# Kernel tuning notes

Measured on AMD Instinct MI355X. Metric: run time of the kernel, lower is better.

Reference implementation:

```python
import jax, jax.numpy as jnp
import numpy as np

N_PTS = 1048576
FEAT = 32
RES = 256


def _sample_plane(plane, gu, gv):
    """Bilinear grid_sample, align_corners=True.
    plane: (C, H, W); gu in [-1,1] indexes W, gv in [-1,1] indexes H.
    Returns (N, C)."""
    C, H, W = plane.shape
    px = (gu + 1.0) * 0.5 * (W - 1)
    py = (gv + 1.0) * 0.5 * (H - 1)
    x0 = jnp.floor(px)
    y0 = jnp.floor(py)
    wx = (px - x0)[None, :]
    wy = (py - y0)[None, :]
    x0i = jnp.clip(x0.astype(jnp.int32), 0, W - 1)
    x1i = jnp.clip(x0i + 1, 0, W - 1)
    y0i = jnp.clip(y0.astype(jnp.int32), 0, H - 1)
    y1i = jnp.clip(y0i + 1, 0, H - 1)
    f00 = plane[:, y0i, x0i]  # (C, N)
    f01 = plane[:, y0i, x1i]
    f10 = plane[:, y1i, x0i]
    f11 = plane[:, y1i, x1i]
    out = (f00 * (1 - wx) * (1 - wy) + f01 * wx * (1 - wy)
           + f10 * (1 - wx) * wy + f11 * wx * wy)
    return out.T  # (N, C)


def setup_inputs() -> dict:
    key = jax.random.key(0)
    ks = jax.random.split(key, 12)
    x = jax.random.uniform(ks[0], (N_PTS, 3), dtype=jnp.float32) * 2.0 - 0.5  # some outside box to exercise clamp
    d = jax.random.normal(ks[1], (N_PTS, 3), dtype=jnp.float32)
    plane_xy = jax.random.normal(ks[2], (FEAT, RES, RES), dtype=jnp.float32)
    plane_xz = jax.random.normal(ks[3], (FEAT, RES, RES), dtype=jnp.float32)
    plane_yz = jax.random.normal(ks[4], (FEAT, RES, RES), dtype=jnp.float32)
    center = jnp.zeros((3,), dtype=jnp.float32)
    scale = jnp.ones((3,), dtype=jnp.float32)
    s = 0.1
    w_sigma1 = jax.random.normal(ks[5], (3 * FEAT, 64), dtype=jnp.float32) * s
    w_sigma2 = jax.random.normal(ks[6], (64, 16), dtype=jnp.float32) * s
    w_color1 = jax.random.normal(ks[7], (15, 64), dtype=jnp.float32) * s
    w_color2 = jax.random.normal(ks[8], (64, 64), dtype=jnp.float32) * s
    w_color3 = jax.random.normal(ks[9], (64, 3), dtype=jnp.float32) * s
    return {"x": x, "d": d, "plane_xy": plane_xy, "plane_xz": plane_xz,
            "plane_yz": plane_yz, "center": center, "scale": scale,
            "w_sigma1": w_sigma1, "w_sigma2": w_sigma2,
            "w_color1": w_color1, "w_color2": w_color2, "w_color3": w_color3}


def reference(x, d, plane_xy, plane_xz, plane_yz, center, scale,
              w_sigma1, w_sigma2, w_color1, w_color2, w_color3):
    # normalize into unit cube and clamp
    xn = jnp.clip((x - center) / scale + 0.5, 0.0, 1.0)
    g = xn * 2.0 - 1.0  # (N, 3) in [-1, 1]
    gx, gy, gz = g[:, 0], g[:, 1], g[:, 2]
    # torch grid_sample: grid[...,0] indexes W (last dim), grid[...,1] indexes H
    feat_xy = _sample_plane(plane_xy, gx, gy)  # plane (C,resX,resY): W<-x, H<-y
    feat_xz = _sample_plane(plane_xz, gx, gz)
    feat_yz = _sample_plane(plane_yz, gy, gz)
    feat = jnp.concatenate([feat_xy, feat_xz, feat_yz], axis=1)  # (N, 96)
    # sigma net: 96 -> 64 (ReLU) -> 16, no bias (tcnn FullyFusedMLP)
    h = jax.nn.relu(feat @ w_sigma1)
    out16 = h @ w_sigma2  # (N, 16)
    sigma = out16[:, 0]
    # color net: 15 -> 64 -> 64 (ReLU) -> 3, sigmoid output
    c = jax.nn.relu(out16[:, 1:] @ w_color1)
    c = jax.nn.relu(c @ w_color2)
    color = jax.nn.sigmoid(c @ w_color3)
    return color, sigma
```

## Files before the change

kernel.cpp:

```cpp
#include <hip/hip_runtime.h>
#include <stdint.h>

typedef __attribute__((ext_vector_type(8))) unsigned short ushort8v;
typedef __attribute__((ext_vector_type(8))) short bf16x8;
typedef __attribute__((ext_vector_type(4))) float f32x4;
typedef __attribute__((ext_vector_type(2))) float f32x2;
typedef __attribute__((ext_vector_type(4))) unsigned int uint4v;

__device__ __forceinline__ float bf2f(unsigned short u) {
    return __uint_as_float(((unsigned)u) << 16);
}
__device__ __forceinline__ unsigned short f2bf(float f) {
    unsigned u = __float_as_uint(f);
    unsigned r = u + 0x7fffu + ((u >> 16) & 1u);
    return (unsigned short)(r >> 16);
}
__device__ __forceinline__ unsigned cvt_pk_bf16(float lo, float hi) {
    unsigned r;
    asm("v_cvt_pk_bf16_f32 %0, %1, %2" : "=v"(r) : "v"(lo), "v"(hi));
    return r;
}
__device__ __forceinline__ f32x2 up2(unsigned u) {
    f32x2 r;
    r[0] = __uint_as_float(u << 16);
    r[1] = __uint_as_float(u & 0xffff0000u);
    return r;
}

__global__ __launch_bounds__(256) void transpose_planes_kernel(
    const float* __restrict__ pxy, const float* __restrict__ pxz,
    const float* __restrict__ pyz, unsigned int* __restrict__ tp)
{
    __shared__ unsigned int lt[64 * 17];
    const int bid = blockIdx.x;
    const int plane = bid >> 10;
    const int base = (bid & 1023) * 64;
    const float* __restrict__ src = plane == 0 ? pxy : (plane == 1 ? pxz : pyz);
    const int tid = threadIdx.x;
    {
        const int c2 = tid >> 4;
        const int s  = tid & 15;
        const f32x4 va = *(const f32x4*)(src + (size_t)(2 * c2)     * 65536 + base + 4 * s);
        const f32x4 vb = *(const f32x4*)(src + (size_t)(2 * c2 + 1) * 65536 + base + 4 * s);
        #pragma unroll
        for (int j = 0; j < 4; ++j) {
            int yx = 4 * s + j;
            lt[yx * 17 + c2] = ((unsigned)f2bf(vb[j]) << 16) | (unsigned)f2bf(va[j]);
        }
    }
    __syncthreads();
    {
        const int yx = tid >> 2, q = tid & 3;
        uint4v o;
        #pragma unroll
        for (int k = 0; k < 4; ++k) o[k] = lt[yx * 17 + 4 * q + k];
        *(uint4v*)(tp + ((size_t)plane * 65536 + base + yx) * 16 + 4 * q) = o;
    }
}

__global__ __launch_bounds__(256) void pack_weights_kernel(
    const float* __restrict__ w1, const float* __restrict__ w2,
    const float* __restrict__ wc1, const float* __restrict__ wc2,
    const float* __restrict__ wc3, unsigned int* __restrict__ pack)
{
    int t = blockIdx.x * 256 + threadIdx.x;
    if (t >= 28 * 64) return;
    int lane = t & 63, tile = t >> 6;
    int mat, mt, kc;
    if (tile < 12)      { mat = 0; kc = tile >> 2;        mt = tile & 3; }
    else if (tile < 14) { mat = 1; kc = tile - 12;        mt = 0; }
    else if (tile < 18) { mat = 2; kc = 0;                mt = tile - 14; }
    else if (tile < 26) { mat = 3; kc = (tile - 18) >> 2; mt = (tile - 18) & 3; }
    else                { mat = 4; kc = tile - 26;        mt = 0; }
    int of = mt * 16 + (lane & 15);
    int kb = kc * 32 + (lane >> 4) * 8;
    float f[8];
    #pragma unroll
    for (int j = 0; j < 8; ++j) {
        int k = kb + j;
        float v;
        if (mat == 0)      v = w1[k * 64 + of];
        else if (mat == 1) v = w2[k * 16 + of];
        else if (mat == 2) v = (k >= 1 && k < 16) ? wc1[(k - 1) * 64 + of] : 0.0f;
        else if (mat == 3) v = wc2[k * 64 + of];
        else               v = (of < 3) ? wc3[k * 3 + of] : 0.0f;
        f[j] = v;
    }
    int sl = lane ^ (lane >> 3);
    unsigned int* dst = pack + tile * 256 + sl * 4;
    #pragma unroll
    for (int w = 0; w < 4; ++w)
        dst[w] = ((unsigned)f2bf(f[2 * w + 1]) << 16) | (unsigned)f2bf(f[2 * w]);
}

__global__ __launch_bounds__(512) void nerf_mfma_kernel(
    const float* __restrict__ xin,
    const unsigned short* __restrict__ tp,
    const unsigned int* __restrict__ wpack,
    const float* __restrict__ center, const float* __restrict__ scale,
    float* __restrict__ out, int npts, int nwt)
{
    __shared__ unsigned int wlds[28 * 256];
    const int tid = threadIdx.x;
    #pragma unroll 2
    for (int idx = tid; idx < 28 * 256; idx += 512) wlds[idx] = wpack[idx];
    __syncthreads();

    const int lane = tid & 63;
    const int wv   = tid >> 6;
    const int p    = lane & 15;
    const int G    = lane >> 4;
    const bool hi32 = (lane & 32) != 0;
    const int sl   = lane ^ (lane >> 3);
    const bf16x8* Af = (const bf16x8*)wlds;

    const float ctr0 = center[0], ctr1 = center[1], ctr2 = center[2];
    const float sc0 = scale[0], sc1 = scale[1], sc2 = scale[2];

    for (int wtb = blockIdx.x * 8; wtb < nwt; wtb += gridDim.x * 8) {
        asm volatile("" ::: "memory");
        const int wt = wtb + wv;
        const int gpt = wt * 16 + p;
        const bool valid = (wt < nwt) && (gpt < npts);
        const int rp = valid ? gpt : (npts - 1);
        const float xv = xin[3 * rp + 0], yv = xin[3 * rp + 1], zv = xin[3 * rp + 2];

        auto norm1 = [&](float v, float c, float s) {
            float xn = fminf(fmaxf((v - c) / s + 0.5f, 0.0f), 1.0f);
            return xn * 2.0f - 1.0f;
        };
        const float gx = norm1(xv, ctr0, sc0);
        const float gy = norm1(yv, ctr1, sc1);
        const float gz = norm1(zv, ctr2, sc2);
        const float us[3] = {gx, gx, gy};
        const float vs[3] = {gy, gz, gz};

        f32x4 acc1[4];
        #pragma unroll
        for (int mt = 0; mt < 4; ++mt) acc1[mt] = f32x4{0.f, 0.f, 0.f, 0.f};
        #pragma unroll
        for (int pl = 0; pl < 3; ++pl) {
            float pxf = (us[pl] + 1.0f) * 0.5f * 255.0f;
            float pyf = (vs[pl] + 1.0f) * 0.5f * 255.0f;
            float x0f = floorf(pxf), y0f = floorf(pyf);
            float wx = pxf - x0f, wy = pyf - y0f;
            int x0 = min(max((int)x0f, 0), 255), y0 = min(max((int)y0f, 0), 255);
            int x1 = min(x0 + 1, 255), y1 = min(y0 + 1, 255);
            float w00 = (1.f - wx) * (1.f - wy), w01 = wx * (1.f - wy);
            float w10 = (1.f - wx) * wy,         w11 = wx * wy;
            const f32x2 W00 = {w00, w00}, W01 = {w01, w01}, W10 = {w10, w10}, W11 = {w11, w11};
            const size_t pbase = ((size_t)pl << 16);
            const uint4v v00 = *(const uint4v*)(tp + (pbase + (size_t)(y0 * 256 + x0)) * 32 + G * 8);
            const uint4v v01 = *(const uint4v*)(tp + (pbase + (size_t)(y0 * 256 + x1)) * 32 + G * 8);
            const uint4v v10 = *(const uint4v*)(tp + (pbase + (size_t)(y1 * 256 + x0)) * 32 + G * 8);
            const uint4v v11 = *(const uint4v*)(tp + (pbase + (size_t)(y1 * 256 + x1)) * 32 + G * 8);
            uint4v bw;
            #pragma unroll
            for (int w = 0; w < 4; ++w) {
                f32x2 a = up2(v00[w]) * W00 + up2(v01[w]) * W01
                        + up2(v10[w]) * W10 + up2(v11[w]) * W11;
                bw[w] = cvt_pk_bf16(a[0], a[1]);
            }
            bf16x8 bfr = __builtin_bit_cast(bf16x8, bw);
            #pragma unroll
            for (int mt = 0; mt < 4; ++mt)
                acc1[mt] = __builtin_amdgcn_mfma_f32_16x16x32_bf16(
                    Af[(pl * 4 + mt) * 64 + sl], bfr, acc1[mt], 0, 0, 0);
        }

        unsigned pk1[4][2];
        #pragma unroll
        for (int mt = 0; mt < 4; ++mt) {
            pk1[mt][0] = cvt_pk_bf16(fmaxf(acc1[mt][0], 0.f), fmaxf(acc1[mt][1], 0.f));
            pk1[mt][1] = cvt_pk_bf16(fmaxf(acc1[mt][2], 0.f), fmaxf(acc1[mt][3], 0.f));
        }
        f32x4 acc2 = f32x4{0.f, 0.f, 0.f, 0.f};
        #pragma unroll
        for (int kc2 = 0; kc2 < 2; ++kc2) {
            uint4v bw;
            #pragma unroll
            for (int w = 0; w < 4; ++w) {
                int src = p + 16 * (2 * (G & 1) + (w >> 1));
                unsigned lo_ = (unsigned)__shfl((int)pk1[2 * kc2][w & 1], src, 64);
                unsigned hi_ = (unsigned)__shfl((int)pk1[2 * kc2 + 1][w & 1], src, 64);
                bw[w] = hi32 ? hi_ : lo_;
            }
            acc2 = __builtin_amdgcn_mfma_f32_16x16x32_bf16(
                Af[(12 + kc2) * 64 + sl], __builtin_bit_cast(bf16x8, bw), acc2, 0, 0, 0);
        }
        if (valid && lane < 16) out[(size_t)3 * npts + gpt] = acc2[0];

        unsigned pk2[2];
        pk2[0] = cvt_pk_bf16(acc2[0], acc2[1]);
        pk2[1] = cvt_pk_bf16(acc2[2], acc2[3]);
        uint4v bw3;
        #pragma unroll
        for (int w = 0; w < 4; ++w) {
            int src = p + 16 * (2 * (G & 1) + (w >> 1));
            unsigned v = (unsigned)__shfl((int)pk2[w & 1], src, 64);
            bw3[w] = (G < 2) ? v : 0u;
        }
        bf16x8 b3 = __builtin_bit_cast(bf16x8, bw3);
        f32x4 acc3[4];
        #pragma unroll
        for (int mt = 0; mt < 4; ++mt) acc3[mt] = f32x4{0.f, 0.f, 0.f, 0.f};
        #pragma unroll
        for (int mt = 0; mt < 4; ++mt)
            acc3[mt] = __builtin_amdgcn_mfma_f32_16x16x32_bf16(
                Af[(14 + mt) * 64 + sl], b3, acc3[mt], 0, 0, 0);

        unsigned pk3[4][2];
        #pragma unroll
        for (int mt = 0; mt < 4; ++mt) {
            pk3[mt][0] = cvt_pk_bf16(fmaxf(acc3[mt][0], 0.f), fmaxf(acc3[mt][1], 0.f));
            pk3[mt][1] = cvt_pk_bf16(fmaxf(acc3[mt][2], 0.f), fmaxf(acc3[mt][3], 0.f));
        }
        f32x4 acc4[4];
        #pragma unroll
        for (int mt = 0; mt < 4; ++mt) acc4[mt] = f32x4{0.f, 0.f, 0.f, 0.f};
        #pragma unroll
        for (int kc2 = 0; kc2 < 2; ++kc2) {
            uint4v bw;
            #pragma unroll
            for (int w = 0; w < 4; ++w) {
                int src = p + 16 * (2 * (G & 1) + (w >> 1));
                unsigned lo_ = (unsigned)__shfl((int)pk3[2 * kc2][w & 1], src, 64);
                unsigned hi_ = (unsigned)__shfl((int)pk3[2 * kc2 + 1][w & 1], src, 64);
                bw[w] = hi32 ? hi_ : lo_;
            }
            bf16x8 b = __builtin_bit_cast(bf16x8, bw);
            #pragma unroll
            for (int mt = 0; mt < 4; ++mt)
                acc4[mt] = __builtin_amdgcn_mfma_f32_16x16x32_bf16(
                    Af[(18 + kc2 * 4 + mt) * 64 + sl], b, acc4[mt], 0, 0, 0);
        }

        unsigned pk4[4][2];
        #pragma unroll
        for (int mt = 0; mt < 4; ++mt) {
            pk4[mt][0] = cvt_pk_bf16(fmaxf(acc4[mt][0], 0.f), fmaxf(acc4[mt][1], 0.f));
            pk4[mt][1] = cvt_pk_bf16(fmaxf(acc4[mt][2], 0.f), fmaxf(acc4[mt][3], 0.f));
        }
        f32x4 acc5 = f32x4{0.f, 0.f, 0.f, 0.f};
        #pragma unroll
        for (int kc2 = 0; kc2 < 2; ++kc2) {
            uint4v bw;
            #pragma unroll
            for (int w = 0; w < 4; ++w) {
                int src = p + 16 * (2 * (G & 1) + (w >> 1));
                unsigned lo_ = (unsigned)__shfl((int)pk4[2 * kc2][w & 1], src, 64);
                unsigned hi_ = (unsigned)__shfl((int)pk4[2 * kc2 + 1][w & 1], src, 64);
                bw[w] = hi32 ? hi_ : lo_;
            }
            acc5 = __builtin_amdgcn_mfma_f32_16x16x32_bf16(
                Af[(26 + kc2) * 64 + sl], __builtin_bit_cast(bf16x8, bw), acc5, 0, 0, 0);
        }
        if (valid && lane < 16) {
            out[(size_t)3 * gpt + 0] = 1.0f / (1.0f + __expf(-acc5[0]));
            out[(size_t)3 * gpt + 1] = 1.0f / (1.0f + __expf(-acc5[1]));
            out[(size_t)3 * gpt + 2] = 1.0f / (1.0f + __expf(-acc5[2]));
        }
    }
}

__global__ __launch_bounds__(256) void nerf_fallback_kernel(
    const float* __restrict__ xin,
    const float* __restrict__ pxy, const float* __restrict__ pxz,
    const float* __restrict__ pyz,
    const float* __restrict__ center, const float* __restrict__ scale,
    const float* __restrict__ w1, const float* __restrict__ w2,
    const float* __restrict__ wc1, const float* __restrict__ wc2,
    const float* __restrict__ wc3, float* __restrict__ out, int npts)
{
    __shared__ unsigned short act[64][256];
    const int tid = threadIdx.x;
    const int i = blockIdx.x * 256 + tid;
    if (i >= npts) return;
    const float xv = xin[3 * i], yv = xin[3 * i + 1], zv = xin[3 * i + 2];
    auto norm1 = [&](float v, int k) {
        float xn = fminf(fmaxf((v - center[k]) / scale[k] + 0.5f, 0.0f), 1.0f);
        return xn * 2.0f - 1.0f;
    };
    const float gx = norm1(xv, 0), gy = norm1(yv, 1), gz = norm1(zv, 2);
    float h[64];
    #pragma unroll
    for (int j = 0; j < 64; ++j) h[j] = 0.0f;
    auto samp = [&](float gu, float gv, int pl, const float* __restrict__ splane) {
        float pxf = (gu + 1.0f) * 0.5f * 255.0f, pyf = (gv + 1.0f) * 0.5f * 255.0f;
        float x0f = floorf(pxf), y0f = floorf(pyf);
        float wx = pxf - x0f, wy = pyf - y0f;
        int x0 = min(max((int)x0f, 0), 255), y0 = min(max((int)y0f, 0), 255);
        int x1 = min(x0 + 1, 255), y1 = min(y0 + 1, 255);
        float w00 = (1 - wx) * (1 - wy), w01 = wx * (1 - wy), w10 = (1 - wx) * wy, w11 = wx * wy;
        for (int c = 0; c < 32; ++c) {
            const float* b = splane + (size_t)c * 65536;
            float f = b[y0 * 256 + x0] * w00 + b[y0 * 256 + x1] * w01
                    + b[y1 * 256 + x0] * w10 + b[y1 * 256 + x1] * w11;
            const float* wr = w1 + (size_t)((pl * 32 + c) * 64);
            #pragma unroll
            for (int j = 0; j < 64; ++j) h[j] = fmaf(f, wr[j], h[j]);
        }
    };
    samp(gx, gy, 0, pxy); samp(gx, gz, 1, pxz); samp(gy, gz, 2, pyz);
    #pragma unroll
    for (int j = 0; j < 64; ++j) act[j][tid] = f2bf(fmaxf(h[j], 0.0f));
    float o[16];
    #pragma unroll
    for (int j = 0; j < 16; ++j) o[j] = 0.0f;
    for (int k = 0; k < 64; ++k) {
        float hv = bf2f(act[k][tid]);
        #pragma unroll
        for (int j = 0; j < 16; ++j) o[j] = fmaf(hv, w2[k * 16 + j], o[j]);
    }
    out[(size_t)3 * npts + i] = o[0];
    float c1[64];
    #pragma unroll
    for (int j = 0; j < 64; ++j) c1[j] = 0.0f;
    #pragma unroll
    for (int k = 0; k < 15; ++k)
        #pragma unroll
        for (int j = 0; j < 64; ++j) c1[j] = fmaf(o[k + 1], wc1[k * 64 + j], c1[j]);
    #pragma unroll
    for (int j = 0; j < 64; ++j) act[j][tid] = f2bf(fmaxf(c1[j], 0.0f));
    float c2[64];
    #pragma unroll
    for (int j = 0; j < 64; ++j) c2[j] = 0.0f;
    for (int k = 0; k < 64; ++k) {
        float v = bf2f(act[k][tid]);
        #pragma unroll
        for (int j = 0; j < 64; ++j) c2[j] = fmaf(v, wc2[k * 64 + j], c2[j]);
    }
    float r0 = 0, r1 = 0, r2 = 0;
    #pragma unroll
    for (int k = 0; k < 64; ++k) {
        float v = fmaxf(c2[k], 0.0f);
        r0 = fmaf(v, wc3[k * 3 + 0], r0);
        r1 = fmaf(v, wc3[k * 3 + 1], r1);
        r2 = fmaf(v, wc3[k * 3 + 2], r2);
    }
    out[(size_t)3 * i + 0] = 1.0f / (1.0f + expf(-r0));
    out[(size_t)3 * i + 1] = 1.0f / (1.0f + expf(-r1));
    out[(size_t)3 * i + 2] = 1.0f / (1.0f + expf(-r2));
}

extern "C" void kernel_launch(void* const* d_in, const int* in_sizes, int n_in,
                              void* d_out, int out_size, void* d_ws, size_t ws_size,
                              hipStream_t stream) {
    const float* x      = (const float*)d_in[0];
    const float* pxy    = (const float*)d_in[2];
    const float* pxz    = (const float*)d_in[3];
    const float* pyz    = (const float*)d_in[4];
    const float* center = (const float*)d_in[5];
    const float* scale  = (const float*)d_in[6];
    const float* w1     = (const float*)d_in[7];
    const float* w2     = (const float*)d_in[8];
    const float* wc1    = (const float*)d_in[9];
    const float* wc2    = (const float*)d_in[10];
    const float* wc3    = (const float*)d_in[11];
    float* out = (float*)d_out;
    const int npts = in_sizes[0] / 3;

    const size_t tp_bytes = (size_t)3 * 256 * 256 * 32 * 2;
    const size_t pack_bytes = 28 * 1024;
    if (ws_size >= tp_bytes + pack_bytes) {
        unsigned int* tp_ws   = (unsigned int*)d_ws;
        unsigned int* pack_ws = (unsigned int*)((char*)d_ws + tp_bytes);
        transpose_planes_kernel<<<3072, 256, 0, stream>>>(pxy, pxz, pyz, tp_ws);
        pack_weights_kernel<<<7, 256, 0, stream>>>(w1, w2, wc1, wc2, wc3, pack_ws);
        const int nwt = (npts + 15) / 16;
        nerf_mfma_kernel<<<1024, 512, 0, stream>>>(
            x, (const unsigned short*)tp_ws, pack_ws, center, scale, out, npts, nwt);
    } else {
        nerf_fallback_kernel<<<(npts + 255) / 256, 256, 0, stream>>>(
            x, pxy, pxz, pyz, center, scale, w1, w2, wc1, wc2, wc3, out, npts);
    }
}
```

Baseline: 187.6 us.

## Process two 16-point tiles per wave to share weight fragments and overlap gathers

Each wave now handles two point tiles per iteration. Every weight fragment read from LDS feeds two MFMAs, and twice as many plane gathers are in flight to hide memory latency. The bilinear index clamps are dropped in favour of fixed byte offsets. At the upper edge this reads a neighbouring texel with zero weight, or past the last plane into the packed-weight area of the workspace. The grid is halved and a min-blocks launch bound is added to limit register pressure, at the cost of fewer resident waves.

```diff
diff --git a/kernel.cpp b/kernel.cpp
--- a/kernel.cpp
+++ b/kernel.cpp
@@ -93,7 +93,7 @@
         dst[w] = ((unsigned)f2bf(f[2 * w + 1]) << 16) | (unsigned)f2bf(f[2 * w]);
 }
 
-__global__ __launch_bounds__(512) void nerf_mfma_kernel(
+__global__ __launch_bounds__(512, 4) void nerf_mfma_kernel(
     const float* __restrict__ xin,
     const unsigned short* __restrict__ tp,
     const unsigned int* __restrict__ wpack,
@@ -113,153 +113,202 @@
     const bool hi32 = (lane & 32) != 0;
     const int sl   = lane ^ (lane >> 3);
     const bf16x8* Af = (const bf16x8*)wlds;
+    const char* tpB = (const char*)tp;
 
     const float ctr0 = center[0], ctr1 = center[1], ctr2 = center[2];
     const float sc0 = scale[0], sc1 = scale[1], sc2 = scale[2];
 
-    for (int wtb = blockIdx.x * 8; wtb < nwt; wtb += gridDim.x * 8) {
+    auto repack64 = [&](const unsigned pk[4][2], int kc2) -> bf16x8 {
+        uint4v bw;
+        #pragma unroll
+        for (int w = 0; w < 4; ++w) {
+            int src = p + 16 * (2 * (G & 1) + (w >> 1));
+            unsigned lo_ = (unsigned)__shfl((int)pk[2 * kc2][w & 1], src, 64);
+            unsigned hi_ = (unsigned)__shfl((int)pk[2 * kc2 + 1][w & 1], src, 64);
+            bw[w] = hi32 ? hi_ : lo_;
+        }
+        return __builtin_bit_cast(bf16x8, bw);
+    };
+
+    for (int wtb = blockIdx.x * 16; wtb < nwt; wtb += gridDim.x * 16) {
         asm volatile("" ::: "memory");
-        const int wt = wtb + wv;
-        const int gpt = wt * 16 + p;
-        const bool valid = (wt < nwt) && (gpt < npts);
-        const int rp = valid ? gpt : (npts - 1);
-        const float xv = xin[3 * rp + 0], yv = xin[3 * rp + 1], zv = xin[3 * rp + 2];
-
-        auto norm1 = [&](float v, float c, float s) {
-            float xn = fminf(fmaxf((v - c) / s + 0.5f, 0.0f), 1.0f);
-            return xn * 2.0f - 1.0f;
-        };
-        const float gx = norm1(xv, ctr0, sc0);
-        const float gy = norm1(yv, ctr1, sc1);
-        const float gz = norm1(zv, ctr2, sc2);
-        const float us[3] = {gx, gx, gy};
-        const float vs[3] = {gy, gz, gz};
-
-        f32x4 acc1[4];
-        #pragma unroll
-        for (int mt = 0; mt < 4; ++mt) acc1[mt] = f32x4{0.f, 0.f, 0.f, 0.f};
+        const int wt0 = wtb + wv * 2;
+        int gpt[2]; bool valid[2];
+        float us[2][3], vs[2][3];
+        #pragma unroll
+        for (int u = 0; u < 2; ++u) {
+            const int wt = wt0 + u;
+            gpt[u] = wt * 16 + p;
+            valid[u] = (wt < nwt) && (gpt[u] < npts);
+            const int rp = valid[u] ? gpt[u] : (npts - 1);
+            const float xv = xin[3 * rp + 0], yv = xin[3 * rp + 1], zv = xin[3 * rp + 2];
+            auto norm1 = [&](float v, float c, float s) {
+                float xn = fminf(fmaxf((v - c) / s + 0.5f, 0.0f), 1.0f);
+                return xn * 2.0f - 1.0f;
+            };
+            const float gx = norm1(xv, ctr0, sc0);
+            const float gy = norm1(yv, ctr1, sc1);
+            const float gz = norm1(zv, ctr2, sc2);
+            us[u][0] = gx; us[u][1] = gx; us[u][2] = gy;
+            vs[u][0] = gy; vs[u][1] = gz; vs[u][2] = gz;
+        }
+
+        f32x4 acc1[2][4];
+        #pragma unroll
+        for (int u = 0; u < 2; ++u)
+            #pragma unroll
+            for (int mt = 0; mt < 4; ++mt) acc1[u][mt] = f32x4{0.f, 0.f, 0.f, 0.f};
+
         #pragma unroll
         for (int pl = 0; pl < 3; ++pl) {
-            float pxf = (us[pl] + 1.0f) * 0.5f * 255.0f;
-            float pyf = (vs[pl] + 1.0f) * 0.5f * 255.0f;
-            float x0f = floorf(pxf), y0f = floorf(pyf);
-            float wx = pxf - x0f, wy = pyf - y0f;
-            int x0 = min(max((int)x0f, 0), 255), y0 = min(max((int)y0f, 0), 255);
-            int x1 = min(x0 + 1, 255), y1 = min(y0 + 1, 255);
-            float w00 = (1.f - wx) * (1.f - wy), w01 = wx * (1.f - wy);
-            float w10 = (1.f - wx) * wy,         w11 = wx * wy;
-            const f32x2 W00 = {w00, w00}, W01 = {w01, w01}, W10 = {w10, w10}, W11 = {w11, w11};
-            const size_t pbase = ((size_t)pl << 16);
-            const uint4v v00 = *(const uint4v*)(tp + (pbase + (size_t)(y0 * 256 + x0)) * 32 + G * 8);
-            const uint4v v01 = *(const uint4v*)(tp + (pbase + (size_t)(y0 * 256 + x1)) * 32 + G * 8);
-            const uint4v v10 = *(const uint4v*)(tp + (pbase + (size_t)(y1 * 256 + x0)) * 32 + G * 8);
-            const uint4v v11 = *(const uint4v*)(tp + (pbase + (size_t)(y1 * 256 + x1)) * 32 + G * 8);
-            uint4v bw;
-            #pragma unroll
-            for (int w = 0; w < 4; ++w) {
-                f32x2 a = up2(v00[w]) * W00 + up2(v01[w]) * W01
-                        + up2(v10[w]) * W10 + up2(v11[w]) * W11;
-                bw[w] = cvt_pk_bf16(a[0], a[1]);
-            }
-            bf16x8 bfr = __builtin_bit_cast(bf16x8, bw);
-            #pragma unroll
-            for (int mt = 0; mt < 4; ++mt)
-                acc1[mt] = __builtin_amdgcn_mfma_f32_16x16x32_bf16(
-                    Af[(pl * 4 + mt) * 64 + sl], bfr, acc1[mt], 0, 0, 0);
-        }
-
-        unsigned pk1[4][2];
-        #pragma unroll
-        for (int mt = 0; mt < 4; ++mt) {
-            pk1[mt][0] = cvt_pk_bf16(fmaxf(acc1[mt][0], 0.f), fmaxf(acc1[mt][1], 0.f));
-            pk1[mt][1] = cvt_pk_bf16(fmaxf(acc1[mt][2], 0.f), fmaxf(acc1[mt][3], 0.f));
-        }
-        f32x4 acc2 = f32x4{0.f, 0.f, 0.f, 0.f};
+            uint4v cv[2][4];
+            float wq[2][4];
+            #pragma unroll
+            for (int u = 0; u < 2; ++u) {
+                float pxf = (us[u][pl] + 1.0f) * 0.5f * 255.0f;
+                float pyf = (vs[u][pl] + 1.0f) * 0.5f * 255.0f;
+                int x0 = (int)pxf, y0 = (int)pyf;
+                float wx = pxf - (float)x0, wy = pyf - (float)y0;
+                wq[u][0] = (1.f - wx) * (1.f - wy); wq[u][1] = wx * (1.f - wy);
+                wq[u][2] = (1.f - wx) * wy;         wq[u][3] = wx * wy;
+                const char* b00 = tpB + (((pl << 16) + (y0 << 8) + x0) << 6) + (G << 4);
+                cv[u][0] = *(const uint4v*)(b00);
+                cv[u][1] = *(const uint4v*)(b00 + 64);
+                cv[u][2] = *(const uint4v*)(b00 + 16384);
+                cv[u][3] = *(const uint4v*)(b00 + 16384 + 64);
+            }
+            bf16x8 bfr[2];
+            #pragma unroll
+            for (int u = 0; u < 2; ++u) {
+                const f32x2 W00 = {wq[u][0], wq[u][0]}, W01 = {wq[u][1], wq[u][1]};
+                const f32x2 W10 = {wq[u][2], wq[u][2]}, W11 = {wq[u][3], wq[u][3]};
+                uint4v bw;
+                #pragma unroll
+                for (int w = 0; w < 4; ++w) {
+                    f32x2 a = up2(cv[u][0][w]) * W00 + up2(cv[u][1][w]) * W01
+                            + up2(cv[u][2][w]) * W10 + up2(cv[u][3][w]) * W11;
+                    bw[w] = cvt_pk_bf16(a[0], a[1]);
+                }
+                bfr[u] = __builtin_bit_cast(bf16x8, bw);
+            }
+            #pragma unroll
+            for (int mt = 0; mt < 4; ++mt) {
+                const bf16x8 frag = Af[(pl * 4 + mt) * 64 + sl];
+                #pragma unroll
+                for (int u = 0; u < 2; ++u)
+                    acc1[u][mt] = __builtin_amdgcn_mfma_f32_16x16x32_bf16(
+                        frag, bfr[u], acc1[u][mt], 0, 0, 0);
+            }
+        }
+
+        unsigned pk1[2][4][2];
+        #pragma unroll
+        for (int u = 0; u < 2; ++u)
+            #pragma unroll
+            for (int mt = 0; mt < 4; ++mt) {
+                pk1[u][mt][0] = cvt_pk_bf16(fmaxf(acc1[u][mt][0], 0.f), fmaxf(acc1[u][mt][1], 0.f));
+                pk1[u][mt][1] = cvt_pk_bf16(fmaxf(acc1[u][mt][2], 0.f), fmaxf(acc1[u][mt][3], 0.f));
+            }
+        f32x4 acc2[2];
+        #pragma unroll
+        for (int u = 0; u < 2; ++u) acc2[u] = f32x4{0.f, 0.f, 0.f, 0.f};
         #pragma unroll
         for (int kc2 = 0; kc2 < 2; ++kc2) {
-            uint4v bw;
+            bf16x8 b[2];
+            #pragma unroll
+            for (int u = 0; u < 2; ++u) b[u] = repack64(pk1[u], kc2);
+            const bf16x8 frag = Af[(12 + kc2) * 64 + sl];
+            #pragma unroll
+            for (int u = 0; u < 2; ++u)
+                acc2[u] = __builtin_amdgcn_mfma_f32_16x16x32_bf16(frag, b[u], acc2[u], 0, 0, 0);
+        }
+        #pragma unroll
+        for (int u = 0; u < 2; ++u)
+            if (valid[u] && lane < 16) out[(size_t)3 * npts + gpt[u]] = acc2[u][0];
+
+        bf16x8 b3[2];
+        #pragma unroll
+        for (int u = 0; u < 2; ++u) {
+            unsigned pk2[2];
+            pk2[0] = cvt_pk_bf16(acc2[u][0], acc2[u][1]);
+            pk2[1] = cvt_pk_bf16(acc2[u][2], acc2[u][3]);
+            uint4v bw3;
             #pragma unroll
             for (int w = 0; w < 4; ++w) {
                 int src = p + 16 * (2 * (G & 1) + (w >> 1));
-                unsigned lo_ = (unsigned)__shfl((int)pk1[2 * kc2][w & 1], src, 64);
-                unsigned hi_ = (unsigned)__shfl((int)pk1[2 * kc2 + 1][w & 1], src, 64);
-                bw[w] = hi32 ? hi_ : lo_;
-            }
-            acc2 = __builtin_amdgcn_mfma_f32_16x16x32_bf16(
-                Af[(12 + kc2) * 64 + sl], __builtin_bit_cast(bf16x8, bw), acc2, 0, 0, 0);
-        }
-        if (valid && lane < 16) out[(size_t)3 * npts + gpt] = acc2[0];
-
-        unsigned pk2[2];
-        pk2[0] = cvt_pk_bf16(acc2[0], acc2[1]);
-        pk2[1] = cvt_pk_bf16(acc2[2], acc2[3]);
-        uint4v bw3;
-        #pragma unroll
-        for (int w = 0; w < 4; ++w) {
-            int src = p + 16 * (2 * (G & 1) + (w >> 1));
-            unsigned v = (unsigned)__shfl((int)pk2[w & 1], src, 64);
-            bw3[w] = (G < 2) ? v : 0u;
-        }
-        bf16x8 b3 = __builtin_bit_cast(bf16x8, bw3);
-        f32x4 acc3[4];
-        #pragma unroll
-        for (int mt = 0; mt < 4; ++mt) acc3[mt] = f32x4{0.f, 0.f, 0.f, 0.f};
-        #pragma unroll
-        for (int mt = 0; mt < 4; ++mt)
-            acc3[mt] = __builtin_amdgcn_mfma_f32_16x16x32_bf16(
-                Af[(14 + mt) * 64 + sl], b3, acc3[mt], 0, 0, 0);
-
-        unsigned pk3[4][2];
+                unsigned v = (unsigned)__shfl((int)pk2[w & 1], src, 64);
+                bw3[w] = (G < 2) ? v : 0u;
+            }
+            b3[u] = __builtin_bit_cast(bf16x8, bw3);
+        }
+        f32x4 acc3[2][4];
+        #pragma unroll
+        for (int u = 0; u < 2; ++u)
+            #pragma unroll
+            for (int mt = 0; mt < 4; ++mt) acc3[u][mt] = f32x4{0.f, 0.f, 0.f, 0.f};
         #pragma unroll
         for (int mt = 0; mt < 4; ++mt) {
-            pk3[mt][0] = cvt_pk_bf16(fmaxf(acc3[mt][0], 0.f), fmaxf(acc3[mt][1], 0.f));
-            pk3[mt][1] = cvt_pk_bf16(fmaxf(acc3[mt][2], 0.f), fmaxf(acc3[mt][3], 0.f));
-        }
-        f32x4 acc4[4];
-        #pragma unroll
-        for (int mt = 0; mt < 4; ++mt) acc4[mt] = f32x4{0.f, 0.f, 0.f, 0.f};
+            const bf16x8 frag = Af[(14 + mt) * 64 + sl];
+            #pragma unroll
+            for (int u = 0; u < 2; ++u)
+                acc3[u][mt] = __builtin_amdgcn_mfma_f32_16x16x32_bf16(frag, b3[u], acc3[u][mt], 0, 0, 0);
+        }
+
+        unsigned pk3[2][4][2];
+        #pragma unroll
+        for (int u = 0; u < 2; ++u)
+            #pragma unroll
+            for (int mt = 0; mt < 4; ++mt) {
+                pk3[u][mt][0] = cvt_pk_bf16(fmaxf(acc3[u][mt][0], 0.f), fmaxf(acc3[u][mt][1], 0.f));
+                pk3[u][mt][1] = cvt_pk_bf16(fmaxf(acc3[u][mt][2], 0.f), fmaxf(acc3[u][mt][3], 0.f));
+            }
+        f32x4 acc4[2][4];
+        #pragma unroll
+        for (int u = 0; u < 2; ++u)
+            #pragma unroll
+            for (int mt = 0; mt < 4; ++mt) acc4[u][mt] = f32x4{0.f, 0.f, 0.f, 0.f};
         #pragma unroll
         for (int kc2 = 0; kc2 < 2; ++kc2) {
-            uint4v bw;
-            #pragma unroll
-            for (int w = 0; w < 4; ++w) {
-                int src = p + 16 * (2 * (G & 1) + (w >> 1));
-                unsigned lo_ = (unsigned)__shfl((int)pk3[2 * kc2][w & 1], src, 64);
-                unsigned hi_ = (unsigned)__shfl((int)pk3[2 * kc2 + 1][w & 1], src, 64);
-                bw[w] = hi32 ? hi_ : lo_;
-            }
-            bf16x8 b = __builtin_bit_cast(bf16x8, bw);
-            #pragma unroll
-            for (int mt = 0; mt < 4; ++mt)
-                acc4[mt] = __builtin_amdgcn_mfma_f32_16x16x32_bf16(
-                    Af[(18 + kc2 * 4 + mt) * 64 + sl], b, acc4[mt], 0, 0, 0);
-        }
-
-        unsigned pk4[4][2];
-        #pragma unroll
-        for (int mt = 0; mt < 4; ++mt) {
-            pk4[mt][0] = cvt_pk_bf16(fmaxf(acc4[mt][0], 0.f), fmaxf(acc4[mt][1], 0.f));
-            pk4[mt][1] = cvt_pk_bf16(fmaxf(acc4[mt][2], 0.f), fmaxf(acc4[mt][3], 0.f));
-        }
-        f32x4 acc5 = f32x4{0.f, 0.f, 0.f, 0.f};
+            bf16x8 b[2];
+            #pragma unroll
+            for (int u = 0; u < 2; ++u) b[u] = repack64(pk3[u], kc2);
+            #pragma unroll
+            for (int mt = 0; mt < 4; ++mt) {
+                const bf16x8 frag = Af[(18 + kc2 * 4 + mt) * 64 + sl];
+                #pragma unroll
+                for (int u = 0; u < 2; ++u)
+                    acc4[u][mt] = __builtin_amdgcn_mfma_f32_16x16x32_bf16(frag, b[u], acc4[u][mt], 0, 0, 0);
+            }
+        }
+
+        unsigned pk4[2][4][2];
+        #pragma unroll
+        for (int u = 0; u < 2; ++u)
+            #pragma unroll
+            for (int mt = 0; mt < 4; ++mt) {
+                pk4[u][mt][0] = cvt_pk_bf16(fmaxf(acc4[u][mt][0], 0.f), fmaxf(acc4[u][mt][1], 0.f));
+                pk4[u][mt][1] = cvt_pk_bf16(fmaxf(acc4[u][mt][2], 0.f), fmaxf(acc4[u][mt][3], 0.f));
+            }
+        f32x4 acc5[2];
+        #pragma unroll
+        for (int u = 0; u < 2; ++u) acc5[u] = f32x4{0.f, 0.f, 0.f, 0.f};
         #pragma unroll
         for (int kc2 = 0; kc2 < 2; ++kc2) {
-            uint4v bw;
-            #pragma unroll
-            for (int w = 0; w < 4; ++w) {
-                int src = p + 16 * (2 * (G & 1) + (w >> 1));
-                unsigned lo_ = (unsigned)__shfl((int)pk4[2 * kc2][w & 1], src, 64);
-                unsigned hi_ = (unsigned)__shfl((int)pk4[2 * kc2 + 1][w & 1], src, 64);
-                bw[w] = hi32 ? hi_ : lo_;
-            }
-            acc5 = __builtin_amdgcn_mfma_f32_16x16x32_bf16(
-                Af[(26 + kc2) * 64 + sl], __builtin_bit_cast(bf16x8, bw), acc5, 0, 0, 0);
-        }
-        if (valid && lane < 16) {
-            out[(size_t)3 * gpt + 0] = 1.0f / (1.0f + __expf(-acc5[0]));
-            out[(size_t)3 * gpt + 1] = 1.0f / (1.0f + __expf(-acc5[1]));
-            out[(size_t)3 * gpt + 2] = 1.0f / (1.0f + __expf(-acc5[2]));
-        }
+            bf16x8 b[2];
+            #pragma unroll
+            for (int u = 0; u < 2; ++u) b[u] = repack64(pk4[u], kc2);
+            const bf16x8 frag = Af[(26 + kc2) * 64 + sl];
+            #pragma unroll
+            for (int u = 0; u < 2; ++u)
+                acc5[u] = __builtin_amdgcn_mfma_f32_16x16x32_bf16(frag, b[u], acc5[u], 0, 0, 0);
+        }
+        #pragma unroll
+        for (int u = 0; u < 2; ++u)
+            if (valid[u] && lane < 16) {
+                out[(size_t)3 * gpt[u] + 0] = 1.0f / (1.0f + __expf(-acc5[u][0]));
+                out[(size_t)3 * gpt[u] + 1] = 1.0f / (1.0f + __expf(-acc5[u][1]));
+                out[(size_t)3 * gpt[u] + 2] = 1.0f / (1.0f + __expf(-acc5[u][2]));
+            }
     }
 }
 
@@ -368,7 +417,7 @@
         transpose_planes_kernel<<<3072, 256, 0, stream>>>(pxy, pxz, pyz, tp_ws);
         pack_weights_kernel<<<7, 256, 0, stream>>>(w1, w2, wc1, wc2, wc3, pack_ws);
         const int nwt = (npts + 15) / 16;
-        nerf_mfma_kernel<<<1024, 512, 0, stream>>>(
+        nerf_mfma_kernel<<<512, 512, 0, stream>>>(
             x, (const unsigned short*)tp_ws, pack_ws, center, scale, out, npts, nwt);
     } else {
         nerf_fallback_kernel<<<(npts + 255) / 256, 256, 0, stream>>>(
```

Result: slower. 193.1 us (+2.9%).
